# Performance work log

Hardware: AMD Instinct MI355X
Metric: run time of the kernel (lower is better)

The kernel has to match this reference:

```python
import jax, jax.numpy as jnp
import numpy as np

DIM, N_HEAD, DK, DV = 1024, 16, 64, 64
B, S = 1, 4096


def setup_inputs() -> dict:
    key = jax.random.key(0)
    ks = jax.random.split(key, 9)
    sd = 0.02
    return {
        "x": jax.random.normal(ks[0], (B, S, DIM), dtype=jnp.float32),
        "Wq": jax.random.normal(ks[1], (DIM, N_HEAD * DK), dtype=jnp.float32) * sd,
        "bq": jnp.zeros((N_HEAD * DK,), dtype=jnp.float32),
        "Wk": jax.random.normal(ks[2], (DIM, N_HEAD * DK), dtype=jnp.float32) * sd,
        "bk": jnp.zeros((N_HEAD * DK,), dtype=jnp.float32),
        "Wv": jax.random.normal(ks[3], (DIM, N_HEAD * DV), dtype=jnp.float32) * sd,
        "bv": jnp.zeros((N_HEAD * DV,), dtype=jnp.float32),
        "Wo": jax.random.normal(ks[4], (N_HEAD * DV, DIM), dtype=jnp.float32) * sd,
        "bo": jnp.zeros((DIM,), dtype=jnp.float32),
    }


def reference(x, Wq, bq, Wk, bk, Wv, bv, Wo, bo):
    b, s, _ = x.shape
    scale = DK ** (-0.5)
    # projections -> [b, h, s, d]
    q = (x @ Wq + bq).reshape(b, s, N_HEAD, DK).transpose(0, 2, 1, 3)
    k = (x @ Wk + bk).reshape(b, s, N_HEAD, DK).transpose(0, 2, 1, 3)
    v = (x @ Wv + bv).reshape(b, s, N_HEAD, DV).transpose(0, 2, 1, 3)
    attn = jnp.einsum("bhqd,bhkd->bhqk", q, k) * scale  # [b,h,s,s]
    attn = jax.nn.softmax(attn, axis=-1)
    out = jnp.einsum("bhqk,bhkd->bhqd", attn, v)  # [b,h,s,dv]
    out = out.transpose(0, 2, 1, 3).reshape(b, s, N_HEAD * DV)
    return out @ Wo + bo
```

## Files before the change

kernel.cpp:

```cpp
#include <hip/hip_runtime.h>
#include <hip/hip_bf16.h>
#include <hip/hip_fp16.h>

#define SEQ 4096
#define DIM 1024
#define NH 16
#define NT (SEQ / 64)

typedef __attribute__((ext_vector_type(4))) float f32x4;
typedef __attribute__((ext_vector_type(8))) _Float16 half8;
typedef __attribute__((ext_vector_type(4))) _Float16 half4;
typedef __attribute__((ext_vector_type(2))) unsigned uint2v;

#if __has_builtin(__builtin_amdgcn_exp2f)
#define EXP2(x) __builtin_amdgcn_exp2f(x)
#else
#define EXP2(x) exp2f(x)
#endif

#define SMC 0.18033688f

__global__ __launch_bounds__(256) void prep_all(const float* __restrict__ x,
                                                _Float16* __restrict__ xh,
                                                const float* __restrict__ W0,
                                                const float* __restrict__ W1,
                                                const float* __restrict__ W2,
                                                const float* __restrict__ W3,
                                                _Float16* __restrict__ T0,
                                                _Float16* __restrict__ T1,
                                                _Float16* __restrict__ T2,
                                                _Float16* __restrict__ T3) {
  if (blockIdx.z == 4) {
    const int blkid = blockIdx.x * 32 + blockIdx.y;
#pragma unroll
    for (int u = 0; u < 4; u++) {
      int i = blkid * 4096 + u * 1024 + threadIdx.x * 4;
      float4 v = *reinterpret_cast<const float4*>(x + i);
      half4 h;
      h[0] = (_Float16)v.x; h[1] = (_Float16)v.y;
      h[2] = (_Float16)v.z; h[3] = (_Float16)v.w;
      *reinterpret_cast<half4*>(xh + i) = h;
    }
    return;
  }
  const float* W = blockIdx.z == 0 ? W0 : blockIdx.z == 1 ? W1 : blockIdx.z == 2 ? W2 : W3;
  _Float16* Wt = blockIdx.z == 0 ? T0 : blockIdx.z == 1 ? T1 : blockIdx.z == 2 ? T2 : T3;
  __shared__ float t[32][33];
  int bx = blockIdx.x * 32;
  int by = blockIdx.y * 32;
  int tx = threadIdx.x & 31, ty = threadIdx.x >> 5;
#pragma unroll
  for (int i = 0; i < 4; i++)
    t[ty + i * 8][tx] = W[(by + ty + i * 8) * DIM + bx + tx];
  __syncthreads();
#pragma unroll
  for (int i = 0; i < 4; i++)
    Wt[(bx + ty + i * 8) * DIM + by + tx] = (_Float16)t[tx][ty + i * 8];
}

template <int MODE>
__device__ __forceinline__ void gemm_body(const _Float16* __restrict__ A,
                                          const _Float16* __restrict__ Bt,
                                          const float* __restrict__ bias,
                                          void* __restrict__ outp,
                                          int M, int N, int Kd, int bmb, int bnb) {
  __shared__ __align__(16) _Float16 As[64][72];
  __shared__ __align__(16) _Float16 Bs[128][72];
  const int tid = threadIdx.x, lane = tid & 63, w = tid >> 6;
  const int bm = bmb * 64, bn = bnb * 128;
  const int l15 = lane & 15, g = lane >> 4, kb = g * 8;
  const int sra = tid >> 2, sca = (tid & 3) * 16;
  const int srb = tid >> 1, scb = (tid & 1) * 32;
  f32x4 acc[4][2] = {};

  uint4 ar0, ar1, br0, br1, br2, br3;
  auto LOADT = [&](int k0) {
    const _Float16* ap = A + (size_t)(bm + sra) * Kd + k0 + sca;
    ar0 = *reinterpret_cast<const uint4*>(ap);
    ar1 = *reinterpret_cast<const uint4*>(ap + 8);
    const _Float16* bp = Bt + (size_t)(bn + srb) * Kd + k0 + scb;
    br0 = *reinterpret_cast<const uint4*>(bp);
    br1 = *reinterpret_cast<const uint4*>(bp + 8);
    br2 = *reinterpret_cast<const uint4*>(bp + 16);
    br3 = *reinterpret_cast<const uint4*>(bp + 24);
  };

  LOADT(0);
  for (int k0 = 0; k0 < Kd; k0 += 64) {
    __syncthreads();
    *reinterpret_cast<uint4*>(&As[sra][sca]) = ar0;
    *reinterpret_cast<uint4*>(&As[sra][sca + 8]) = ar1;
    *reinterpret_cast<uint4*>(&Bs[srb][scb]) = br0;
    *reinterpret_cast<uint4*>(&Bs[srb][scb + 8]) = br1;
    *reinterpret_cast<uint4*>(&Bs[srb][scb + 16]) = br2;
    *reinterpret_cast<uint4*>(&Bs[srb][scb + 24]) = br3;
    __syncthreads();
    if (k0 + 64 < Kd) LOADT(k0 + 64);
#pragma unroll
    for (int kk = 0; kk < 64; kk += 32) {
      half8 af[4], bf[2];
#pragma unroll
      for (int i = 0; i < 4; i++)
        af[i] = *reinterpret_cast<const half8*>(&As[i * 16 + l15][kk + kb]);
#pragma unroll
      for (int j = 0; j < 2; j++)
        bf[j] = *reinterpret_cast<const half8*>(&Bs[w * 32 + j * 16 + l15][kk + kb]);
      __builtin_amdgcn_s_setprio(1);
#pragma unroll
      for (int i = 0; i < 4; i++)
#pragma unroll
        for (int j = 0; j < 2; j++)
          acc[i][j] = __builtin_amdgcn_mfma_f32_16x16x32_f16(af[i], bf[j], acc[i][j], 0, 0, 0);
      __builtin_amdgcn_s_setprio(0);
    }
  }

#pragma unroll
  for (int i = 0; i < 4; i++)
#pragma unroll
    for (int j = 0; j < 2; j++) {
      const int col = bn + w * 32 + j * 16 + l15;
      if (MODE == 2) {
        const int rowP = bm + g * 16 + i * 4;
        half4 hv;
#pragma unroll
        for (int r = 0; r < 4; r++) hv[r] = (_Float16)(acc[i][j][r] + bias[col]);
        *reinterpret_cast<half4*>(&((_Float16*)outp)[(size_t)col * M + rowP]) = hv;
      } else {
        const int row0 = bm + i * 16 + g * 4;
#pragma unroll
        for (int r = 0; r < 4; r++) {
          float vv = acc[i][j][r] + bias[col];
          if (MODE == 0) {
            _Float16* O = (_Float16*)outp;
            O[(((col >> 6) * SEQ) + row0 + r) * 64 + (col & 63)] = (_Float16)vv;
          } else {
            float* O = (float*)outp;
            O[(size_t)(row0 + r) * N + col] = vv;
          }
        }
      }
    }
}

__global__ __launch_bounds__(256) void gemm_qkv(const _Float16* __restrict__ A,
                                                const _Float16* __restrict__ WqT,
                                                const _Float16* __restrict__ WkT,
                                                const _Float16* __restrict__ WvT,
                                                const float* __restrict__ bq,
                                                const float* __restrict__ bk,
                                                const float* __restrict__ bv,
                                                _Float16* __restrict__ Qd,
                                                _Float16* __restrict__ Kd,
                                                _Float16* __restrict__ Vd) {
  if (blockIdx.z == 0)
    gemm_body<0>(A, WqT, bq, (void*)Qd, SEQ, DIM, DIM, blockIdx.x, blockIdx.y);
  else if (blockIdx.z == 1)
    gemm_body<0>(A, WkT, bk, (void*)Kd, SEQ, DIM, DIM, blockIdx.x, blockIdx.y);
  else
    gemm_body<2>(A, WvT, bv, (void*)Vd, SEQ, DIM, DIM, blockIdx.x, blockIdx.y);
}

__global__ __launch_bounds__(256) void gemm_out(const _Float16* __restrict__ A,
                                                const _Float16* __restrict__ Bt,
                                                const float* __restrict__ bias,
                                                float* __restrict__ out) {
  gemm_body<1>(A, Bt, bias, (void*)out, SEQ, DIM, DIM, blockIdx.x, blockIdx.y);
}

__global__ __launch_bounds__(256) void attn_fwd(const _Float16* __restrict__ Q,
                                                const _Float16* __restrict__ Kh,
                                                const _Float16* __restrict__ Vt_g,
                                                _Float16* __restrict__ Og) {
  __shared__ __align__(16) _Float16 Ks[3][64][72];
  __shared__ __align__(16) _Float16 Vs[3][64][72];
  __shared__ __align__(16) _Float16 Ps[4][2][16][72];
  const int h = blockIdx.y;
  const int q0 = blockIdx.x * 128;
  const int tid = threadIdx.x, lane = tid & 63, w = tid >> 6;
  const int l15 = lane & 15, g = lane >> 4, kb = g * 8;

  const int qrow = q0 + w * 32 + l15;
  const _Float16* qp = Q + ((size_t)h * SEQ + qrow) * 64;
  half8 qf[2][2];
  qf[0][0] = *reinterpret_cast<const half8*>(qp + kb);
  qf[0][1] = *reinterpret_cast<const half8*>(qp + 32 + kb);
  qf[1][0] = *reinterpret_cast<const half8*>(qp + 16 * 64 + kb);
  qf[1][1] = *reinterpret_cast<const half8*>(qp + 16 * 64 + 32 + kb);

  f32x4 o[2][4] = {};
  f32x4 ol[2] = {};
  float m[2] = {-1e30f, -1e30f};
  float negmC[2] = {1e30f, 1e30f};

  const f32x4 kZero = {0.f, 0.f, 0.f, 0.f};
  const _Float16 one1 = (_Float16)1.f;
  const half8 kOnes8 = {one1, one1, one1, one1, one1, one1, one1, one1};

  const int srow = tid >> 3, sc8 = (tid & 7) * 8;
  const _Float16* kbase = Kh + (size_t)h * SEQ * 64;
  const _Float16* vbase = Vt_g + (size_t)h * 64 * SEQ;

  uint4 kr0, kr1, vr0, vr1;
  auto LOADKV = [&](int kt2) {
    const _Float16* kp = kbase + (size_t)(kt2 * 64 + srow) * 64 + sc8;
    kr0 = *reinterpret_cast<const uint4*>(kp);
    kr1 = *reinterpret_cast<const uint4*>(kp + 32 * 64);
    const _Float16* vp = vbase + (size_t)srow * SEQ + kt2 * 64 + sc8;
    vr0 = *reinterpret_cast<const uint4*>(vp);
    vr1 = *reinterpret_cast<const uint4*>(vp + 32 * SEQ);
  };
  auto STAGE = [&](int buf) {
    *reinterpret_cast<uint4*>(&Ks[buf][srow][sc8]) = kr0;
    *reinterpret_cast<uint4*>(&Ks[buf][srow + 32][sc8]) = kr1;
    *reinterpret_cast<uint4*>(&Vs[buf][srow][sc8]) = vr0;
    *reinterpret_cast<uint4*>(&Vs[buf][srow + 32][sc8]) = vr1;
  };

  auto QK = [&](int tile, f32x4 (&sf)[2][4]) {
    const int b = tile % 3;
    __builtin_amdgcn_s_setprio(1);
#pragma unroll
    for (int f = 0; f < 4; f++) {
      half8 kf0 = *reinterpret_cast<const half8*>(&Ks[b][f * 16 + l15][kb]);
      half8 kf1 = *reinterpret_cast<const half8*>(&Ks[b][f * 16 + l15][32 + kb]);
      sf[0][f] = __builtin_amdgcn_mfma_f32_16x16x32_f16(kf0, qf[0][0], kZero, 0, 0, 0);
      sf[0][f] = __builtin_amdgcn_mfma_f32_16x16x32_f16(kf1, qf[0][1], sf[0][f], 0, 0, 0);
      sf[1][f] = __builtin_amdgcn_mfma_f32_16x16x32_f16(kf0, qf[1][0], kZero, 0, 0, 0);
      sf[1][f] = __builtin_amdgcn_mfma_f32_16x16x32_f16(kf1, qf[1][1], sf[1][f], 0, 0, 0);
    }
    __builtin_amdgcn_s_setprio(0);
  };

  auto ITER = [&](int t, f32x4 (&scur)[2][4], f32x4 (&snext)[2][4]) {
    if (t + 1 < NT) QK(t + 1, snext);

#pragma unroll
    for (int s = 0; s < 2; s++) {
      float m0 = fmaxf(fmaxf(scur[s][0][0], scur[s][0][1]), scur[s][0][2]);
      float m1 = fmaxf(fmaxf(scur[s][0][3], scur[s][1][0]), scur[s][1][1]);
      float m2 = fmaxf(fmaxf(scur[s][1][2], scur[s][1][3]), scur[s][2][0]);
      float m3 = fmaxf(fmaxf(scur[s][2][1], scur[s][2][2]), scur[s][2][3]);
      float m4 = fmaxf(fmaxf(scur[s][3][0], scur[s][3][1]), scur[s][3][2]);
      float pm = fmaxf(fmaxf(fmaxf(m0, m1), m2), fmaxf(fmaxf(m3, m4), scur[s][3][3]));
      if (__any(pm > m[s] + 64.f)) {
        pm = fmaxf(pm, __shfl_xor(pm, 16, 64));
        pm = fmaxf(pm, __shfl_xor(pm, 32, 64));
        float mn = fmaxf(m[s], pm);
        float al = EXP2((m[s] - mn) * SMC);
        m[s] = mn;
        negmC[s] = -mn * SMC;
        ol[s] *= al;
#pragma unroll
        for (int f = 0; f < 4; f++) o[s][f] *= al;
      }
      unsigned us[8];
#pragma unroll
      for (int f = 0; f < 4; f++) {
        float p0 = EXP2(fmaf(scur[s][f][0], SMC, negmC[s]));
        float p1 = EXP2(fmaf(scur[s][f][1], SMC, negmC[s]));
        float p2 = EXP2(fmaf(scur[s][f][2], SMC, negmC[s]));
        float p3 = EXP2(fmaf(scur[s][f][3], SMC, negmC[s]));
        us[2 * f] = __builtin_bit_cast(unsigned, __builtin_amdgcn_cvt_pkrtz(p0, p1));
        us[2 * f + 1] = __builtin_bit_cast(unsigned, __builtin_amdgcn_cvt_pkrtz(p2, p3));
      }
      uint4 w0 = {us[0], us[1], us[2], us[3]};
      uint4 w1 = {us[4], us[5], us[6], us[7]};
      *reinterpret_cast<uint4*>(&Ps[w][s][l15][g * 16]) = w0;
      *reinterpret_cast<uint4*>(&Ps[w][s][l15][g * 16 + 8]) = w1;
    }

    half8 pa[2][2];
#pragma unroll
    for (int s = 0; s < 2; s++) {
      pa[s][0] = *reinterpret_cast<const half8*>(&Ps[w][s][l15][kb]);
      pa[s][1] = *reinterpret_cast<const half8*>(&Ps[w][s][l15][32 + kb]);
    }

    const int bv = t % 3;
    __builtin_amdgcn_s_setprio(1);
#pragma unroll
    for (int f = 0; f < 4; f++) {
      half8 vf0 = *reinterpret_cast<const half8*>(&Vs[bv][f * 16 + l15][kb]);
      half8 vf1 = *reinterpret_cast<const half8*>(&Vs[bv][f * 16 + l15][32 + kb]);
      o[0][f] = __builtin_amdgcn_mfma_f32_16x16x32_f16(vf0, pa[0][0], o[0][f], 0, 0, 0);
      o[0][f] = __builtin_amdgcn_mfma_f32_16x16x32_f16(vf1, pa[0][1], o[0][f], 0, 0, 0);
      o[1][f] = __builtin_amdgcn_mfma_f32_16x16x32_f16(vf0, pa[1][0], o[1][f], 0, 0, 0);
      o[1][f] = __builtin_amdgcn_mfma_f32_16x16x32_f16(vf1, pa[1][1], o[1][f], 0, 0, 0);
    }
    ol[0] = __builtin_amdgcn_mfma_f32_16x16x32_f16(kOnes8, pa[0][0], ol[0], 0, 0, 0);
    ol[0] = __builtin_amdgcn_mfma_f32_16x16x32_f16(kOnes8, pa[0][1], ol[0], 0, 0, 0);
    ol[1] = __builtin_amdgcn_mfma_f32_16x16x32_f16(kOnes8, pa[1][0], ol[1], 0, 0, 0);
    ol[1] = __builtin_amdgcn_mfma_f32_16x16x32_f16(kOnes8, pa[1][1], ol[1], 0, 0, 0);
    __builtin_amdgcn_s_setprio(0);

    if (t + 2 < NT) STAGE((t + 2) % 3);
    if (t + 3 < NT) LOADKV(t + 3);
    __syncthreads();
  };

  LOADKV(0); STAGE(0);
  LOADKV(1); STAGE(1);
  LOADKV(2);
  __syncthreads();

  f32x4 sfA[2][4], sfB[2][4];
  QK(0, sfA);
  for (int t = 0; t < NT; t += 2) {
    ITER(t, sfA, sfB);
    ITER(t + 1, sfB, sfA);
  }

#pragma unroll
  for (int s = 0; s < 2; s++) {
    float rinv = 1.f / ol[s][0];
#pragma unroll
    for (int f = 0; f < 4; f++) {
      half4 hv;
#pragma unroll
      for (int r = 0; r < 4; r++) hv[r] = (_Float16)(o[s][f][r] * rinv);
      *reinterpret_cast<half4*>(
          &Og[(size_t)(qrow + 16 * s) * DIM + h * 64 + f * 16 + g * 4]) = hv;
    }
  }
}


extern "C" void kernel_launch(void* const* d_in, const int* in_sizes, int n_in,
                              void* d_out, int out_size, void* d_ws, size_t ws_size,
                              hipStream_t stream) {
  const float* x  = (const float*)d_in[0];
  const float* Wq = (const float*)d_in[1];
  const float* bq = (const float*)d_in[2];
  const float* Wk = (const float*)d_in[3];
  const float* bk = (const float*)d_in[4];
  const float* Wv = (const float*)d_in[5];
  const float* bv = (const float*)d_in[6];
  const float* Wo = (const float*)d_in[7];
  const float* bo = (const float*)d_in[8];

  char* ws = (char*)d_ws;
  _Float16* xh  = (_Float16*)ws;
  _Float16* WqT = (_Float16*)(ws + (size_t)SEQ * DIM * 2);
  _Float16* WkT = WqT + DIM * DIM;
  _Float16* WvT = WkT + DIM * DIM;
  _Float16* WoT = WvT + DIM * DIM;
  _Float16* Qd  = WoT + DIM * DIM;
  _Float16* Kd  = Qd + (size_t)SEQ * DIM;
  _Float16* Vd  = Kd + (size_t)SEQ * DIM;
  _Float16* Od  = Vd + (size_t)SEQ * DIM;

  prep_all<<<dim3(32, 32, 5), 256, 0, stream>>>(x, xh, Wq, Wk, Wv, Wo,
                                                WqT, WkT, WvT, WoT);

  gemm_qkv<<<dim3(SEQ / 64, DIM / 128, 3), 256, 0, stream>>>(
      xh, WqT, WkT, WvT, bq, bk, bv, Qd, Kd, Vd);

  attn_fwd<<<dim3(SEQ / 128, NH), 256, 0, stream>>>(Qd, Kd, Vd, Od);

  gemm_out<<<dim3(SEQ / 64, DIM / 128), 256, 0, stream>>>(Od, WoT, bo, (float*)d_out);
}
```

Before: 176.1 us.

## Load K/V tiles directly into LDS with XOR-swizzled unpadded layout

Replaces the register-staged K/V prefetch (global load into VGPRs, later store to padded LDS) with `global_load_lds` DMA that writes straight into shared memory two tiles ahead. Since LDS DMA needs contiguous rows, the padding is dropped and an XOR swizzle on the 16-byte chunk index is applied both when loading and when reading fragments, to avoid bank conflicts. This is meant to remove the LDS store instructions and free staging registers. The risk is that the barrier may now wait on the just-issued DMA, which shortens the effective prefetch overlap.

```diff
diff --git a/kernel.cpp b/kernel.cpp
--- a/kernel.cpp
+++ b/kernel.cpp
@@ -11,6 +11,9 @@
 typedef __attribute__((ext_vector_type(8))) _Float16 half8;
 typedef __attribute__((ext_vector_type(4))) _Float16 half4;
 typedef __attribute__((ext_vector_type(2))) unsigned uint2v;
+
+typedef const unsigned __attribute__((address_space(1)))* gas_t;
+typedef unsigned __attribute__((address_space(3)))* las_t;
 
 #if __has_builtin(__builtin_amdgcn_exp2f)
 #define EXP2(x) __builtin_amdgcn_exp2f(x)
@@ -172,13 +175,16 @@
                                                 const _Float16* __restrict__ Kh,
                                                 const _Float16* __restrict__ Vt_g,
                                                 _Float16* __restrict__ Og) {
-  __shared__ __align__(16) _Float16 Ks[3][64][72];
-  __shared__ __align__(16) _Float16 Vs[3][64][72];
+  __shared__ __align__(16) _Float16 Ks[3][64][64];
+  __shared__ __align__(16) _Float16 Vs[3][64][64];
   __shared__ __align__(16) _Float16 Ps[4][2][16][72];
   const int h = blockIdx.y;
   const int q0 = blockIdx.x * 128;
   const int tid = threadIdx.x, lane = tid & 63, w = tid >> 6;
   const int l15 = lane & 15, g = lane >> 4, kb = g * 8;
+  const int sw = l15 & 7;
+  const int c0 = ((g ^ sw) * 8);
+  const int c1 = (((4 + g) ^ sw) * 8);
 
   const int qrow = q0 + w * 32 + l15;
   const _Float16* qp = Q + ((size_t)h * SEQ + qrow) * 64;
@@ -197,24 +203,24 @@
   const _Float16 one1 = (_Float16)1.f;
   const half8 kOnes8 = {one1, one1, one1, one1, one1, one1, one1, one1};
 
-  const int srow = tid >> 3, sc8 = (tid & 7) * 8;
   const _Float16* kbase = Kh + (size_t)h * SEQ * 64;
   const _Float16* vbase = Vt_g + (size_t)h * 64 * SEQ;
 
-  uint4 kr0, kr1, vr0, vr1;
-  auto LOADKV = [&](int kt2) {
-    const _Float16* kp = kbase + (size_t)(kt2 * 64 + srow) * 64 + sc8;
-    kr0 = *reinterpret_cast<const uint4*>(kp);
-    kr1 = *reinterpret_cast<const uint4*>(kp + 32 * 64);
-    const _Float16* vp = vbase + (size_t)srow * SEQ + kt2 * 64 + sc8;
-    vr0 = *reinterpret_cast<const uint4*>(vp);
-    vr1 = *reinterpret_cast<const uint4*>(vp + 32 * SEQ);
-  };
-  auto STAGE = [&](int buf) {
-    *reinterpret_cast<uint4*>(&Ks[buf][srow][sc8]) = kr0;
-    *reinterpret_cast<uint4*>(&Ks[buf][srow + 32][sc8]) = kr1;
-    *reinterpret_cast<uint4*>(&Vs[buf][srow][sc8]) = vr0;
-    *reinterpret_cast<uint4*>(&Vs[buf][srow + 32][sc8]) = vr1;
+  const int lrow = lane >> 3;
+  const int lchk = (lane & 7) ^ lrow;
+  auto GLDS = [&](int kt2) {
+    const int b = kt2 % 3;
+    const int r0 = w * 16;
+    const _Float16* ks0 = kbase + ((size_t)kt2 * 64 + r0 + lrow) * 64 + lchk * 8;
+    __builtin_amdgcn_global_load_lds((gas_t)(const void*)ks0,
+                                     (las_t)(void*)&Ks[b][r0][0], 16, 0, 0);
+    __builtin_amdgcn_global_load_lds((gas_t)(const void*)(ks0 + 8 * 64),
+                                     (las_t)(void*)&Ks[b][r0 + 8][0], 16, 0, 0);
+    const _Float16* vs0 = vbase + (size_t)(r0 + lrow) * SEQ + kt2 * 64 + lchk * 8;
+    __builtin_amdgcn_global_load_lds((gas_t)(const void*)vs0,
+                                     (las_t)(void*)&Vs[b][r0][0], 16, 0, 0);
+    __builtin_amdgcn_global_load_lds((gas_t)(const void*)(vs0 + 8 * SEQ),
+                                     (las_t)(void*)&Vs[b][r0 + 8][0], 16, 0, 0);
   };
 
   auto QK = [&](int tile, f32x4 (&sf)[2][4]) {
@@ -222,8 +228,8 @@
     __builtin_amdgcn_s_setprio(1);
 #pragma unroll
     for (int f = 0; f < 4; f++) {
-      half8 kf0 = *reinterpret_cast<const half8*>(&Ks[b][f * 16 + l15][kb]);
-      half8 kf1 = *reinterpret_cast<const half8*>(&Ks[b][f * 16 + l15][32 + kb]);
+      half8 kf0 = *reinterpret_cast<const half8*>(&Ks[b][f * 16 + l15][c0]);
+      half8 kf1 = *reinterpret_cast<const half8*>(&Ks[b][f * 16 + l15][c1]);
       sf[0][f] = __builtin_amdgcn_mfma_f32_16x16x32_f16(kf0, qf[0][0], kZero, 0, 0, 0);
       sf[0][f] = __builtin_amdgcn_mfma_f32_16x16x32_f16(kf1, qf[0][1], sf[0][f], 0, 0, 0);
       sf[1][f] = __builtin_amdgcn_mfma_f32_16x16x32_f16(kf0, qf[1][0], kZero, 0, 0, 0);
@@ -233,6 +239,7 @@
   };
 
   auto ITER = [&](int t, f32x4 (&scur)[2][4], f32x4 (&snext)[2][4]) {
+    if (t + 2 < NT) GLDS(t + 2);
     if (t + 1 < NT) QK(t + 1, snext);
 
 #pragma unroll
@@ -281,8 +288,8 @@
     __builtin_amdgcn_s_setprio(1);
 #pragma unroll
     for (int f = 0; f < 4; f++) {
-      half8 vf0 = *reinterpret_cast<const half8*>(&Vs[bv][f * 16 + l15][kb]);
-      half8 vf1 = *reinterpret_cast<const half8*>(&Vs[bv][f * 16 + l15][32 + kb]);
+      half8 vf0 = *reinterpret_cast<const half8*>(&Vs[bv][f * 16 + l15][c0]);
+      half8 vf1 = *reinterpret_cast<const half8*>(&Vs[bv][f * 16 + l15][c1]);
       o[0][f] = __builtin_amdgcn_mfma_f32_16x16x32_f16(vf0, pa[0][0], o[0][f], 0, 0, 0);
       o[0][f] = __builtin_amdgcn_mfma_f32_16x16x32_f16(vf1, pa[0][1], o[0][f], 0, 0, 0);
       o[1][f] = __builtin_amdgcn_mfma_f32_16x16x32_f16(vf0, pa[1][0], o[1][f], 0, 0, 0);
@@ -294,14 +301,11 @@
     ol[1] = __builtin_amdgcn_mfma_f32_16x16x32_f16(kOnes8, pa[1][1], ol[1], 0, 0, 0);
     __builtin_amdgcn_s_setprio(0);
 
-    if (t + 2 < NT) STAGE((t + 2) % 3);
-    if (t + 3 < NT) LOADKV(t + 3);
     __syncthreads();
   };
 
-  LOADKV(0); STAGE(0);
-  LOADKV(1); STAGE(1);
-  LOADKV(2);
+  GLDS(0);
+  GLDS(1);
   __syncthreads();
 
   f32x4 sfA[2][4], sfB[2][4];
```

After: 180.6 us. 1.03x slower.

## Switch attention to 32x32x16 MFMA and keep P in registers

Applied to the files above, without the earlier changes.

Rewrites the attention inner loop to use 32x32x16 MFMA tiles instead of 16x16x32. With that layout the softmax probabilities come out of the QK product already in the register layout the PV MFMA needs, so the LDS round trip through the Ps buffer is removed. The row-sum is now accumulated with scalar adds plus one cross-lane shuffle instead of extra MFMAs against a ones vector. The V-projection store layout is permuted to match the new K-dimension ordering. In exchange the kernel carries larger accumulator register blocks, which may lower occupancy.

```diff
diff --git a/kernel.cpp b/kernel.cpp
--- a/kernel.cpp
+++ b/kernel.cpp
@@ -8,9 +8,9 @@
 #define NT (SEQ / 64)
 
 typedef __attribute__((ext_vector_type(4))) float f32x4;
+typedef __attribute__((ext_vector_type(16))) float f32x16;
 typedef __attribute__((ext_vector_type(8))) _Float16 half8;
 typedef __attribute__((ext_vector_type(4))) _Float16 half4;
-typedef __attribute__((ext_vector_type(2))) unsigned uint2v;
 
 #if __has_builtin(__builtin_amdgcn_exp2f)
 #define EXP2(x) __builtin_amdgcn_exp2f(x)
@@ -115,13 +115,14 @@
     }
   }
 
+  const int gswap = ((g & 1) << 1) | (g >> 1);
 #pragma unroll
   for (int i = 0; i < 4; i++)
 #pragma unroll
     for (int j = 0; j < 2; j++) {
       const int col = bn + w * 32 + j * 16 + l15;
       if (MODE == 2) {
-        const int rowP = bm + g * 16 + i * 4;
+        const int rowP = bm + i * 16 + gswap * 4;
         half4 hv;
 #pragma unroll
         for (int r = 0; r < 4; r++) hv[r] = (_Float16)(acc[i][j][r] + bias[col]);
@@ -174,32 +175,25 @@
                                                 _Float16* __restrict__ Og) {
   __shared__ __align__(16) _Float16 Ks[3][64][72];
   __shared__ __align__(16) _Float16 Vs[3][64][72];
-  __shared__ __align__(16) _Float16 Ps[4][2][16][72];
-  const int h = blockIdx.y;
+  const int hh = blockIdx.y;
   const int q0 = blockIdx.x * 128;
   const int tid = threadIdx.x, lane = tid & 63, w = tid >> 6;
-  const int l15 = lane & 15, g = lane >> 4, kb = g * 8;
-
-  const int qrow = q0 + w * 32 + l15;
-  const _Float16* qp = Q + ((size_t)h * SEQ + qrow) * 64;
-  half8 qf[2][2];
-  qf[0][0] = *reinterpret_cast<const half8*>(qp + kb);
-  qf[0][1] = *reinterpret_cast<const half8*>(qp + 32 + kb);
-  qf[1][0] = *reinterpret_cast<const half8*>(qp + 16 * 64 + kb);
-  qf[1][1] = *reinterpret_cast<const half8*>(qp + 16 * 64 + 32 + kb);
-
-  f32x4 o[2][4] = {};
-  f32x4 ol[2] = {};
-  float m[2] = {-1e30f, -1e30f};
-  float negmC[2] = {1e30f, 1e30f};
-
-  const f32x4 kZero = {0.f, 0.f, 0.f, 0.f};
-  const _Float16 one1 = (_Float16)1.f;
-  const half8 kOnes8 = {one1, one1, one1, one1, one1, one1, one1, one1};
+  const int l31 = lane & 31, hq = lane >> 5, h8 = hq * 8;
+
+  const int qrow = q0 + w * 32 + l31;
+  const _Float16* qp = Q + ((size_t)hh * SEQ + qrow) * 64;
+  half8 qf[4];
+#pragma unroll
+  for (int d = 0; d < 4; d++)
+    qf[d] = *reinterpret_cast<const half8*>(qp + d * 16 + h8);
+
+  f32x16 o[2] = {};
+  float m = -1e30f, lsum = 0.f, negmC = 1e30f;
+  const f32x16 kZero16 = {};
 
   const int srow = tid >> 3, sc8 = (tid & 7) * 8;
-  const _Float16* kbase = Kh + (size_t)h * SEQ * 64;
-  const _Float16* vbase = Vt_g + (size_t)h * 64 * SEQ;
+  const _Float16* kbase = Kh + (size_t)hh * SEQ * 64;
+  const _Float16* vbase = Vt_g + (size_t)hh * 64 * SEQ;
 
   uint4 kr0, kr1, vr0, vr1;
   auto LOADKV = [&](int kt2) {
@@ -217,81 +211,85 @@
     *reinterpret_cast<uint4*>(&Vs[buf][srow + 32][sc8]) = vr1;
   };
 
-  auto QK = [&](int tile, f32x4 (&sf)[2][4]) {
+  auto QK = [&](int tile, f32x16 (&sf)[2]) {
     const int b = tile % 3;
     __builtin_amdgcn_s_setprio(1);
-#pragma unroll
-    for (int f = 0; f < 4; f++) {
-      half8 kf0 = *reinterpret_cast<const half8*>(&Ks[b][f * 16 + l15][kb]);
-      half8 kf1 = *reinterpret_cast<const half8*>(&Ks[b][f * 16 + l15][32 + kb]);
-      sf[0][f] = __builtin_amdgcn_mfma_f32_16x16x32_f16(kf0, qf[0][0], kZero, 0, 0, 0);
-      sf[0][f] = __builtin_amdgcn_mfma_f32_16x16x32_f16(kf1, qf[0][1], sf[0][f], 0, 0, 0);
-      sf[1][f] = __builtin_amdgcn_mfma_f32_16x16x32_f16(kf0, qf[1][0], kZero, 0, 0, 0);
-      sf[1][f] = __builtin_amdgcn_mfma_f32_16x16x32_f16(kf1, qf[1][1], sf[1][f], 0, 0, 0);
+    {
+      half8 kf0 = *reinterpret_cast<const half8*>(&Ks[b][l31][h8]);
+      half8 kf1 = *reinterpret_cast<const half8*>(&Ks[b][32 + l31][h8]);
+      sf[0] = __builtin_amdgcn_mfma_f32_32x32x16_f16(kf0, qf[0], kZero16, 0, 0, 0);
+      sf[1] = __builtin_amdgcn_mfma_f32_32x32x16_f16(kf1, qf[0], kZero16, 0, 0, 0);
+    }
+#pragma unroll
+    for (int d = 1; d < 4; d++) {
+      half8 kf0 = *reinterpret_cast<const half8*>(&Ks[b][l31][d * 16 + h8]);
+      half8 kf1 = *reinterpret_cast<const half8*>(&Ks[b][32 + l31][d * 16 + h8]);
+      sf[0] = __builtin_amdgcn_mfma_f32_32x32x16_f16(kf0, qf[d], sf[0], 0, 0, 0);
+      sf[1] = __builtin_amdgcn_mfma_f32_32x32x16_f16(kf1, qf[d], sf[1], 0, 0, 0);
     }
     __builtin_amdgcn_s_setprio(0);
   };
 
-  auto ITER = [&](int t, f32x4 (&scur)[2][4], f32x4 (&snext)[2][4]) {
+  auto ITER = [&](int t, f32x16 (&scur)[2], f32x16 (&snext)[2]) {
     if (t + 1 < NT) QK(t + 1, snext);
 
-#pragma unroll
-    for (int s = 0; s < 2; s++) {
-      float m0 = fmaxf(fmaxf(scur[s][0][0], scur[s][0][1]), scur[s][0][2]);
-      float m1 = fmaxf(fmaxf(scur[s][0][3], scur[s][1][0]), scur[s][1][1]);
-      float m2 = fmaxf(fmaxf(scur[s][1][2], scur[s][1][3]), scur[s][2][0]);
-      float m3 = fmaxf(fmaxf(scur[s][2][1], scur[s][2][2]), scur[s][2][3]);
-      float m4 = fmaxf(fmaxf(scur[s][3][0], scur[s][3][1]), scur[s][3][2]);
-      float pm = fmaxf(fmaxf(fmaxf(m0, m1), m2), fmaxf(fmaxf(m3, m4), scur[s][3][3]));
-      if (__any(pm > m[s] + 64.f)) {
-        pm = fmaxf(pm, __shfl_xor(pm, 16, 64));
-        pm = fmaxf(pm, __shfl_xor(pm, 32, 64));
-        float mn = fmaxf(m[s], pm);
-        float al = EXP2((m[s] - mn) * SMC);
-        m[s] = mn;
-        negmC[s] = -mn * SMC;
-        ol[s] *= al;
-#pragma unroll
-        for (int f = 0; f < 4; f++) o[s][f] *= al;
+    float pm = scur[0][0];
+#pragma unroll
+    for (int r = 1; r < 16; r++) pm = fmaxf(pm, scur[0][r]);
+#pragma unroll
+    for (int r = 0; r < 16; r++) pm = fmaxf(pm, scur[1][r]);
+    if (__any(pm > m + 64.f)) {
+      pm = fmaxf(pm, __shfl_xor(pm, 32, 64));
+      float mn = fmaxf(m, pm);
+      float al = EXP2((m - mn) * SMC);
+      m = mn;
+      negmC = -mn * SMC;
+      lsum *= al;
+      o[0] *= al;
+      o[1] *= al;
+    }
+    f32x16 pf0, pf1;
+#pragma unroll
+    for (int r = 0; r < 16; r++) {
+      float p = EXP2(fmaf(scur[0][r], SMC, negmC));
+      pf0[r] = p;
+      lsum += p;
+    }
+#pragma unroll
+    for (int r = 0; r < 16; r++) {
+      float p = EXP2(fmaf(scur[1][r], SMC, negmC));
+      pf1[r] = p;
+      lsum += p;
+    }
+    half8 pb[4];
+#pragma unroll
+    for (int s = 0; s < 4; s++) {
+      const int base = (s & 1) * 8;
+      unsigned d0, d1, d2, d3;
+      if (s < 2) {
+        d0 = __builtin_bit_cast(unsigned, __builtin_amdgcn_cvt_pkrtz(pf0[base + 0], pf0[base + 1]));
+        d1 = __builtin_bit_cast(unsigned, __builtin_amdgcn_cvt_pkrtz(pf0[base + 2], pf0[base + 3]));
+        d2 = __builtin_bit_cast(unsigned, __builtin_amdgcn_cvt_pkrtz(pf0[base + 4], pf0[base + 5]));
+        d3 = __builtin_bit_cast(unsigned, __builtin_amdgcn_cvt_pkrtz(pf0[base + 6], pf0[base + 7]));
+      } else {
+        d0 = __builtin_bit_cast(unsigned, __builtin_amdgcn_cvt_pkrtz(pf1[base + 0], pf1[base + 1]));
+        d1 = __builtin_bit_cast(unsigned, __builtin_amdgcn_cvt_pkrtz(pf1[base + 2], pf1[base + 3]));
+        d2 = __builtin_bit_cast(unsigned, __builtin_amdgcn_cvt_pkrtz(pf1[base + 4], pf1[base + 5]));
+        d3 = __builtin_bit_cast(unsigned, __builtin_amdgcn_cvt_pkrtz(pf1[base + 6], pf1[base + 7]));
       }
-      unsigned us[8];
-#pragma unroll
-      for (int f = 0; f < 4; f++) {
-        float p0 = EXP2(fmaf(scur[s][f][0], SMC, negmC[s]));
-        float p1 = EXP2(fmaf(scur[s][f][1], SMC, negmC[s]));
-        float p2 = EXP2(fmaf(scur[s][f][2], SMC, negmC[s]));
-        float p3 = EXP2(fmaf(scur[s][f][3], SMC, negmC[s]));
-        us[2 * f] = __builtin_bit_cast(unsigned, __builtin_amdgcn_cvt_pkrtz(p0, p1));
-        us[2 * f + 1] = __builtin_bit_cast(unsigned, __builtin_amdgcn_cvt_pkrtz(p2, p3));
-      }
-      uint4 w0 = {us[0], us[1], us[2], us[3]};
-      uint4 w1 = {us[4], us[5], us[6], us[7]};
-      *reinterpret_cast<uint4*>(&Ps[w][s][l15][g * 16]) = w0;
-      *reinterpret_cast<uint4*>(&Ps[w][s][l15][g * 16 + 8]) = w1;
-    }
-
-    half8 pa[2][2];
-#pragma unroll
-    for (int s = 0; s < 2; s++) {
-      pa[s][0] = *reinterpret_cast<const half8*>(&Ps[w][s][l15][kb]);
-      pa[s][1] = *reinterpret_cast<const half8*>(&Ps[w][s][l15][32 + kb]);
+      uint4 uu = {d0, d1, d2, d3};
+      pb[s] = __builtin_bit_cast(half8, uu);
     }
 
     const int bv = t % 3;
     __builtin_amdgcn_s_setprio(1);
 #pragma unroll
-    for (int f = 0; f < 4; f++) {
-      half8 vf0 = *reinterpret_cast<const half8*>(&Vs[bv][f * 16 + l15][kb]);
-      half8 vf1 = *reinterpret_cast<const half8*>(&Vs[bv][f * 16 + l15][32 + kb]);
-      o[0][f] = __builtin_amdgcn_mfma_f32_16x16x32_f16(vf0, pa[0][0], o[0][f], 0, 0, 0);
-      o[0][f] = __builtin_amdgcn_mfma_f32_16x16x32_f16(vf1, pa[0][1], o[0][f], 0, 0, 0);
-      o[1][f] = __builtin_amdgcn_mfma_f32_16x16x32_f16(vf0, pa[1][0], o[1][f], 0, 0, 0);
-      o[1][f] = __builtin_amdgcn_mfma_f32_16x16x32_f16(vf1, pa[1][1], o[1][f], 0, 0, 0);
-    }
-    ol[0] = __builtin_amdgcn_mfma_f32_16x16x32_f16(kOnes8, pa[0][0], ol[0], 0, 0, 0);
-    ol[0] = __builtin_amdgcn_mfma_f32_16x16x32_f16(kOnes8, pa[0][1], ol[0], 0, 0, 0);
-    ol[1] = __builtin_amdgcn_mfma_f32_16x16x32_f16(kOnes8, pa[1][0], ol[1], 0, 0, 0);
-    ol[1] = __builtin_amdgcn_mfma_f32_16x16x32_f16(kOnes8, pa[1][1], ol[1], 0, 0, 0);
+    for (int s = 0; s < 4; s++) {
+      half8 va0 = *reinterpret_cast<const half8*>(&Vs[bv][l31][s * 16 + h8]);
+      half8 va1 = *reinterpret_cast<const half8*>(&Vs[bv][32 + l31][s * 16 + h8]);
+      o[0] = __builtin_amdgcn_mfma_f32_32x32x16_f16(va0, pb[s], o[0], 0, 0, 0);
+      o[1] = __builtin_amdgcn_mfma_f32_32x32x16_f16(va1, pb[s], o[1], 0, 0, 0);
+    }
     __builtin_amdgcn_s_setprio(0);
 
     if (t + 2 < NT) STAGE((t + 2) % 3);
@@ -304,25 +302,25 @@
   LOADKV(2);
   __syncthreads();
 
-  f32x4 sfA[2][4], sfB[2][4];
+  f32x16 sfA[2], sfB[2];
   QK(0, sfA);
   for (int t = 0; t < NT; t += 2) {
     ITER(t, sfA, sfB);
     ITER(t + 1, sfB, sfA);
   }
 
-#pragma unroll
-  for (int s = 0; s < 2; s++) {
-    float rinv = 1.f / ol[s][0];
-#pragma unroll
-    for (int f = 0; f < 4; f++) {
+  float ls = lsum + __shfl_xor(lsum, 32, 64);
+  float rinv = 1.f / ls;
+#pragma unroll
+  for (int tile = 0; tile < 2; tile++)
+#pragma unroll
+    for (int rg = 0; rg < 4; rg++) {
       half4 hv;
 #pragma unroll
-      for (int r = 0; r < 4; r++) hv[r] = (_Float16)(o[s][f][r] * rinv);
-      *reinterpret_cast<half4*>(
-          &Og[(size_t)(qrow + 16 * s) * DIM + h * 64 + f * 16 + g * 4]) = hv;
-    }
-  }
+      for (int j = 0; j < 4; j++) hv[j] = (_Float16)(o[tile][rg * 4 + j] * rinv);
+      const int dv = tile * 32 + rg * 8 + 4 * hq;
+      *reinterpret_cast<half4*>(&Og[(size_t)qrow * DIM + hh * 64 + dv]) = hv;
+    }
 }
 
 
```

After: 171.1 us. 1.03x faster.
